# Kernel tuning notes

Hardware: AMD Instinct MI355X
Metric: run time of the kernel (lower is better)

Reference implementation:

```python
import jax, jax.numpy as jnp
import numpy as np

DIM = 1024
NUM_HEADS = 16
HEAD_DIM = DIM // NUM_HEADS


def apply_rotary_embed(x, thetas):
    # x: (..., seq, d), thetas: (seq, d) broadcast over leading dims
    x1, x2 = jnp.split(x, 2, axis=-1)
    x_rot = jnp.concatenate([-x2, x1], axis=-1)
    return x * jnp.cos(thetas) + x_rot * jnp.sin(thetas)


def setup_inputs() -> dict:
    key = jax.random.key(0)
    ks = jax.random.split(key, 8)
    B, Nx, Nc = 4, 1024, 2048
    x = jax.random.normal(ks[0], (B, Nx, DIM), dtype=jnp.float32)
    c = jax.random.normal(ks[1], (B, Nc, DIM), dtype=jnp.float32)
    x_pos_embed = jax.random.normal(ks[2], (Nx, HEAD_DIM), dtype=jnp.float32)
    c_pos_embed = jax.random.normal(ks[3], (Nc, HEAD_DIM), dtype=jnp.float32)
    s = 1.0 / np.sqrt(DIM)
    Wq = jax.random.normal(ks[4], (DIM, DIM), dtype=jnp.float32) * s
    Wkv = jax.random.normal(ks[5], (DIM, 2 * DIM), dtype=jnp.float32) * s
    Wproj = jax.random.normal(ks[6], (DIM, DIM), dtype=jnp.float32) * s
    bproj = jnp.zeros((DIM,), dtype=jnp.float32)
    return {"x": x, "c": c, "x_pos_embed": x_pos_embed, "c_pos_embed": c_pos_embed,
            "Wq": Wq, "Wkv": Wkv, "Wproj": Wproj, "bproj": bproj}


def reference(x, c, x_pos_embed, c_pos_embed, Wq, Wkv, Wproj, bproj):
    B, Nx, D = x.shape
    Nc = c.shape[1]
    H, hd = NUM_HEADS, HEAD_DIM
    # Q projection -> (B, H, Nx, hd)
    q = (x @ Wq).reshape(B, Nx, H, hd).transpose(0, 2, 1, 3)
    q = apply_rotary_embed(q, x_pos_embed)
    # KV projection -> k, v each (B, H, Nc, hd)
    kv = (c @ Wkv).reshape(B, Nc, 2, H, hd).transpose(2, 0, 3, 1, 4)
    k, v = kv[0], kv[1]
    k = apply_rotary_embed(k, c_pos_embed)
    # scaled dot-product attention (dropout p=0 -> identity)
    scale = 1.0 / np.sqrt(hd).astype(np.float32)
    attn = jnp.einsum('bhqd,bhkd->bhqk', q, k) * scale
    attn = jax.nn.softmax(attn, axis=-1)
    out = jnp.einsum('bhqk,bhkd->bhqd', attn, v)
    out = out.transpose(0, 2, 1, 3).reshape(B, Nx, D)
    return out @ Wproj + bproj
```

## Files before the change

kernel.cpp:

```cpp
#include <hip/hip_runtime.h>
#include <math.h>

#define DIMC  1024
#define NHEAD 16
#define HD    64
#define NB    4
#define NX    1024
#define NC    2048
#define KD    1024

typedef _Float16 half_t;
typedef __attribute__((ext_vector_type(8))) _Float16 h8;
typedef __attribute__((ext_vector_type(4))) _Float16 h4;
typedef __attribute__((ext_vector_type(2))) __fp16 fp16x2;
typedef __attribute__((ext_vector_type(4))) float f32x4;

#define QSCALE 0.1803368801111244f
#define NEGM  -8.656170245333781f

__device__ __forceinline__ void gload_lds16(const half_t* g, half_t* l) {
    __builtin_amdgcn_global_load_lds(
        (__attribute__((address_space(1))) void*)(g),
        (__attribute__((address_space(3))) void*)(l), 16, 0, 0);
}

__device__ __forceinline__ void wtile(const float* __restrict__ W,
                                      half_t* __restrict__ Wt, int N, int IMG,
                                      int bx, int by, int t)
{
    __shared__ half_t T[64][72];
    const int k0 = by * 64, n0 = bx * 64;
    const int kr = t >> 2, c0 = (t & 3) << 4;
    const float* src = W + (size_t)(k0 + kr) * N + n0 + c0;
#pragma unroll
    for (int j = 0; j < 16; j += 4) {
        float4 v = *(const float4*)(src + j);
        T[c0 + j + 0][kr] = (half_t)v.x;
        T[c0 + j + 1][kr] = (half_t)v.y;
        T[c0 + j + 2][kr] = (half_t)v.z;
        T[c0 + j + 3][kr] = (half_t)v.w;
    }
    __syncthreads();
    const int nr = t >> 2, kc = (t & 3) << 4;
    if (!IMG) {
        half_t* dst = Wt + (size_t)(n0 + nr) * KD + k0 + kc;
        *(int4*)dst       = *(const int4*)&T[nr][kc];
        *(int4*)(dst + 8) = *(const int4*)&T[nr][kc + 8];
    } else {
        const int n = n0 + nr;
        const int ntile = n >> 8, rr = n & 255;
        const int s0 = kc >> 3;
        half_t* base = Wt + ((size_t)(ntile * 16 + by) * 256 + rr) * 64;
        *(int4*)(base + ((s0 ^ (rr & 7)) << 3))       = *(const int4*)&T[nr][kc];
        *(int4*)(base + (((s0 + 1) ^ (rr & 7)) << 3)) = *(const int4*)&T[nr][kc + 8];
    }
}

__global__ __launch_bounds__(256) void prep(
    const float* __restrict__ x, half_t* __restrict__ xh,
    const float* __restrict__ c, half_t* __restrict__ ch,
    const float* __restrict__ xpe, const float* __restrict__ cpe,
    float* __restrict__ xct, float* __restrict__ xst,
    float* __restrict__ cct, float* __restrict__ cst,
    const float* __restrict__ Wq,  half_t* __restrict__ Wqt,
    const float* __restrict__ Wkv, half_t* __restrict__ Wkt,
    const float* __restrict__ Wp,  half_t* __restrict__ Wpt)
{
    const int bid = blockIdx.x, t = threadIdx.x;
    if (bid < 1024) {
        if (bid < 256)      wtile(Wq,  Wqt, DIMC, 0,     bid & 15,         bid >> 4,         t);
        else if (bid < 768) wtile(Wkv, Wkt, 2 * DIMC, 1, (bid - 256) & 31, (bid - 256) >> 5, t);
        else                wtile(Wp,  Wpt, DIMC, 0,     (bid - 768) & 15, (bid - 768) >> 4, t);
    } else if (bid < 7168) {
        const int nx = NB * NX * DIMC;
        const int i = ((bid - 1024) * 256 + t) * 8;
        const float* s;
        h8 o;
        if (i < nx) {
            s = x + i;
            float4 a = *(const float4*)(s);
            float4 b = *(const float4*)(s + 4);
            o[0] = (half_t)a.x; o[1] = (half_t)a.y; o[2] = (half_t)a.z; o[3] = (half_t)a.w;
            o[4] = (half_t)b.x; o[5] = (half_t)b.y; o[6] = (half_t)b.z; o[7] = (half_t)b.w;
            *(h8*)(xh + i) = o;
        } else {
            const int j = i - nx;
            s = c + j;
            float4 a = *(const float4*)(s);
            float4 b = *(const float4*)(s + 4);
            o[0] = (half_t)a.x; o[1] = (half_t)a.y; o[2] = (half_t)a.z; o[3] = (half_t)a.w;
            o[4] = (half_t)b.x; o[5] = (half_t)b.y; o[6] = (half_t)b.z; o[7] = (half_t)b.w;
            const int R = j >> 10, k = j & 1023;
            const int mt = R >> 8, r = R & 255, kt = k >> 6, sl = (k & 63) >> 3;
            *(h8*)(ch + ((size_t)(mt * 16 + kt) * 256 + r) * 64 + ((sl ^ (r & 7)) << 3)) = o;
        }
    } else {
        const int i = (bid - 7168) * 256 + t;
        if (i < NX * HD) {
            const float th = xpe[i];
            xct[i] = cosf(th); xst[i] = sinf(th);
        } else {
            const int j = i - NX * HD;
            const float th = cpe[j];
            cct[j] = cosf(th); cst[j] = sinf(th);
        }
    }
}

template <int MODE, int BN>
__global__ __launch_bounds__(256) void hgemm(
    const half_t* __restrict__ Ag, const half_t* __restrict__ Bt,
    const float* __restrict__ ct, const float* __restrict__ st,
    const float* __restrict__ bias,
    void* __restrict__ out0, void* __restrict__ out1)
{
    constexpr int MI = (BN == 128) ? 4 : 2;
    constexpr int BLOADS = BN / 32;
    __shared__ half_t As[2][8192];
    __shared__ half_t Bs[2][BN * 64];

    const int tid = threadIdx.x;
    const int w = tid >> 6, lane = tid & 63;
    const int lr = lane & 15, lg = lane >> 4;
    const int wrOff = (BN == 128) ? (w >> 1) * 64 : w * 32;
    const int wcOff = (BN == 128) ? (w & 1) * 64 : 0;

    int lin = (int)blockIdx.x;
    lin = (lin & 7) * ((int)gridDim.x >> 3) + (lin >> 3);
    const int m0 = (lin >> 4) * 128, n0 = (lin & 15) * BN;

    f32x4 acc[MI][4];
#pragma unroll
    for (int i = 0; i < MI; ++i)
#pragma unroll
        for (int j = 0; j < 4; ++j) acc[i][j] = f32x4{0.f, 0.f, 0.f, 0.f};

    size_t gA[4], gB[BLOADS];
    int loff[4];
#pragma unroll
    for (int c = 0; c < 4; ++c) {
        const int L = c * 4096 + w * 1024 + lane * 16;
        const int row = L >> 7;
        const int ss = ((L >> 4) & 7) ^ (row & 7);
        gA[c] = (size_t)(m0 + row) * KD + ss * 8;
        if (c < BLOADS) gB[c] = (size_t)(n0 + row) * KD + ss * 8;
        loff[c] = c * 2048 + w * 512;
    }

#define HSTAGE(buf, kk) do {                                               \
        _Pragma("unroll")                                                  \
        for (int c = 0; c < 4; ++c) {                                      \
            gload_lds16(Ag + gA[c] + (kk) * 64, &As[buf][loff[c]]);        \
            if (c < BLOADS) gload_lds16(Bt + gB[c] + (kk) * 64, &Bs[buf][loff[c]]); \
        }                                                                  \
    } while (0)

    HSTAGE(0, 0);
    asm volatile("s_waitcnt vmcnt(0)" ::: "memory");
    __builtin_amdgcn_s_barrier();
    __builtin_amdgcn_sched_barrier(0);

    for (int k = 0; k < KD / 64; ++k) {
        const int cb = k & 1;
        if (k + 1 < KD / 64) {
            HSTAGE(cb ^ 1, k + 1);
            if constexpr (BLOADS == 4)
                asm volatile("s_waitcnt vmcnt(8)" ::: "memory");
            else
                asm volatile("s_waitcnt vmcnt(6)" ::: "memory");
        } else {
            asm volatile("s_waitcnt vmcnt(0)" ::: "memory");
        }
        __builtin_amdgcn_s_barrier();
        __builtin_amdgcn_sched_barrier(0);

        __builtin_amdgcn_s_setprio(1);
#pragma unroll
        for (int kc = 0; kc < 2; ++kc) {
            h8 af[MI], bf[4];
#pragma unroll
            for (int mi = 0; mi < MI; ++mi) {
                const int r = wrOff + mi * 16 + lr;
                af[mi] = *(const h8*)&As[cb][r * 64 + (((kc * 4 + lg) ^ (r & 7)) << 3)];
            }
#pragma unroll
            for (int ni = 0; ni < 4; ++ni) {
                const int r = wcOff + ni * 16 + lr;
                bf[ni] = *(const h8*)&Bs[cb][r * 64 + (((kc * 4 + lg) ^ (r & 7)) << 3)];
            }
#pragma unroll
            for (int mi = 0; mi < MI; ++mi)
#pragma unroll
                for (int ni = 0; ni < 4; ++ni)
                    acc[mi][ni] = __builtin_amdgcn_mfma_f32_16x16x32_f16(
                        af[mi], bf[ni], acc[mi][ni], 0, 0, 0);
        }
        __builtin_amdgcn_s_setprio(0);

        __builtin_amdgcn_s_barrier();
        __builtin_amdgcn_sched_barrier(0);
    }
#undef HSTAGE

    if (MODE == 2) {
        float* o = (float*)out0;
#pragma unroll
        for (int ni = 0; ni < 4; ++ni) {
            const int col = n0 + ni * 16 + lr;
            const float bv = bias[col];
#pragma unroll
            for (int mi = 0; mi < MI; ++mi)
#pragma unroll
                for (int r = 0; r < 4; ++r) {
                    const int row = m0 + wrOff + mi * 16 + lg * 4 + r;
                    o[(size_t)row * DIMC + col] = acc[mi][ni][r] + bv;
                }
        }
        return;
    }

    if (MODE == 0) {
        half_t* Qw = (half_t*)out0;
        const int h = n0 >> 6;
#pragma unroll
        for (int mi = 0; mi < MI; ++mi)
#pragma unroll
            for (int r = 0; r < 4; ++r) {
                const int row = m0 + wrOff + mi * 16 + lg * 4 + r;
                const int bb = row >> 10, nn = row & (NX - 1);
                const float* cr = ct + nn * HD;
                const float* sr = st + nn * HD;
                half_t* op = Qw + (((size_t)(bb * NHEAD + h)) * NX + nn) * HD;
#pragma unroll
                for (int ni = 0; ni < 4; ++ni) {
                    const int d = ni * 16 + lr;
                    const float val = acc[mi][ni][r];
                    const float pv  = acc[mi][ni ^ 2][r];
                    op[d] = (half_t)((val * cr[d] + (ni < 2 ? -pv : pv) * sr[d]) * QSCALE);
                }
            }
    }
}

__global__ __launch_bounds__(512, 2) void hgemm_kv(
    const half_t* __restrict__ Aimg, const half_t* __restrict__ Bimg,
    const float* __restrict__ ct, const float* __restrict__ st,
    half_t* __restrict__ Kw, half_t* __restrict__ Vw)
{
    __shared__ half_t lds[65536];

    const int tid = threadIdx.x;
    const int w = tid >> 6, lane = tid & 63;
    const int lr = lane & 15, lg = lane >> 4;
    const int wr = w >> 2, wc = w & 3;
    const int wrOff = wr * 128, wcOff = wc * 64;

    int lin = (int)blockIdx.x;
    lin = (lin & 7) * 32 + (lin >> 3);
    const int mt = lin >> 3, nt = lin & 7;
    const int m0 = mt * 256, n0 = nt * 256;

    const half_t* Ablk = Aimg + (size_t)mt * 262144;
    const half_t* Bblk = Bimg + (size_t)nt * 262144;
    const int so2 = w * 512 + lane * 8;

    f32x4 acc[8][4];
#pragma unroll
    for (int i = 0; i < 8; ++i)
#pragma unroll
        for (int j = 0; j < 4; ++j) acc[i][j] = f32x4{0.f, 0.f, 0.f, 0.f};
    h8 af[2][2];
    h8 bf[4][2];

#define ISSUEH(SRC, DSTOFF) do {                                     \
        gload_lds16((SRC) + so2,        &lds[(DSTOFF) + w * 512]);   \
        gload_lds16((SRC) + 4096 + so2, &lds[(DSTOFF) + 4096 + w * 512]); \
    } while (0)

#define PHASE(MI0, AOFF, BOFF, READBF, STG, GATE) do {               \
        _Pragma("unroll")                                            \
        for (int kc = 0; kc < 2; ++kc)                               \
        _Pragma("unroll")                                            \
        for (int d = 0; d < 2; ++d) {                                \
            const int r_ = wrOff + ((MI0) + d) * 16 + lr;            \
            af[d][kc] = *(const h8*)&lds[(AOFF) + r_ * 64 + (((kc * 4 + lg) ^ (r_ & 7)) << 3)]; \
        }                                                            \
        if (READBF) {                                                \
            _Pragma("unroll")                                        \
            for (int ni = 0; ni < 4; ++ni)                           \
            _Pragma("unroll")                                        \
            for (int kc = 0; kc < 2; ++kc) {                         \
                const int rb = wcOff + ni * 16 + lr;                 \
                bf[ni][kc] = *(const h8*)&lds[(BOFF) + rb * 64 + (((kc * 4 + lg) ^ (rb & 7)) << 3)]; \
            }                                                        \
        }                                                            \
        STG;                                                         \
        __builtin_amdgcn_sched_barrier(0);                           \
        __builtin_amdgcn_s_barrier();                                \
        __builtin_amdgcn_s_setprio(1);                               \
        _Pragma("unroll")                                            \
        for (int d = 0; d < 2; ++d)                                  \
        _Pragma("unroll")                                            \
        for (int ni = 0; ni < 4; ++ni)                               \
        _Pragma("unroll")                                            \
        for (int kc = 0; kc < 2; ++kc)                               \
            acc[(MI0) + d][ni] = __builtin_amdgcn_mfma_f32_16x16x32_f16( \
                af[d][kc], bf[ni][kc], acc[(MI0) + d][ni], 0, 0, 0); \
        __builtin_amdgcn_s_setprio(0);                               \
        GATE;                                                        \
        __builtin_amdgcn_s_barrier();                                \
    } while (0)

#define GATE4 asm volatile("s_waitcnt vmcnt(4)" ::: "memory")
#define GATE0 asm volatile("s_waitcnt vmcnt(0)" ::: "memory")
#define NOG   ((void)0)

    ISSUEH(Ablk, 0);          ISSUEH(Ablk + 8192, 8192);
    ISSUEH(Bblk, 32768);      ISSUEH(Bblk + 8192, 32768 + 8192);
    __builtin_amdgcn_sched_barrier(0);
    ISSUEH(Bblk + 16384, 49152); ISSUEH(Bblk + 16384 + 8192, 49152 + 8192);
    asm volatile("s_waitcnt vmcnt(4)" ::: "memory");
    __builtin_amdgcn_s_barrier();

    for (int i = 0; i < 7; ++i) {
        const half_t* An1 = Ablk + (size_t)(2 * i + 1) * 16384;
        const half_t* An2 = Ablk + (size_t)(2 * i + 2) * 16384;
        const half_t* Bn2 = Bblk + (size_t)(2 * i + 2) * 16384;
        const half_t* Bn3 = Bblk + (size_t)(2 * i + 3) * 16384;
        PHASE(0, 0,     32768, true,  ISSUEH(An1, 16384),               NOG);
        PHASE(2, 0,     32768, false, ISSUEH(An1 + 8192, 16384 + 8192), NOG);
        PHASE(4, 0,     32768, false, ISSUEH(Bn2, 32768),               NOG);
        PHASE(6, 0,     32768, false, ISSUEH(Bn2 + 8192, 32768 + 8192), GATE4);
        PHASE(0, 16384, 49152, true,  ISSUEH(An2, 0),                   NOG);
        PHASE(2, 16384, 49152, false, ISSUEH(An2 + 8192, 8192),         NOG);
        PHASE(4, 16384, 49152, false, ISSUEH(Bn3, 49152),               NOG);
        PHASE(6, 16384, 49152, false, ISSUEH(Bn3 + 8192, 49152 + 8192), GATE4);
    }
    {
        const half_t* A15 = Ablk + (size_t)15 * 16384;
        PHASE(0, 0,     32768, true,  ISSUEH(A15, 16384),               NOG);
        PHASE(2, 0,     32768, false, ISSUEH(A15 + 8192, 16384 + 8192), NOG);
        PHASE(4, 0,     32768, false, NOG,                              NOG);
        PHASE(6, 0,     32768, false, NOG,                              GATE0);
        PHASE(0, 16384, 49152, true,  NOG,                              NOG);
        PHASE(2, 16384, 49152, false, NOG,                              NOG);
        PHASE(4, 16384, 49152, false, NOG,                              NOG);
        PHASE(6, 16384, 49152, false, NOG,                              NOG);
    }
#undef PHASE
#undef ISSUEH
#undef GATE4
#undef GATE0
#undef NOG

    const bool isK = (n0 < DIMC);
    const int h = ((n0 & (DIMC - 1)) >> 6) + wc;
#pragma unroll
    for (int mi = 0; mi < 8; ++mi)
#pragma unroll
        for (int r = 0; r < 4; ++r) {
            const int row = m0 + wrOff + mi * 16 + lg * 4 + r;
            const int bb = row >> 11, nn = row & (NC - 1);
            const int tt = nn >> 6, rr = nn & 63;
            const size_t tbase = ((size_t)(bb * NHEAD + h) * 32 + tt) * 4096;
            const float* cr = ct + nn * HD;
            const float* sr = st + nn * HD;
#pragma unroll
            for (int ni = 0; ni < 4; ++ni) {
                const int d = ni * 16 + lr;
                const float val = acc[mi][ni][r];
                if (isK) {
                    const float pv = acc[mi][ni ^ 2][r];
                    Kw[tbase + rr * 64 + ((((d >> 3) ^ (rr & 7)) << 3) | (d & 7))] =
                        (half_t)(val * cr[d] + (ni < 2 ? -pv : pv) * sr[d]);
                } else {
                    Vw[tbase + d * 64 + ((((rr >> 3) ^ (d & 7)) << 3) | (rr & 7))] =
                        (half_t)val;
                }
            }
        }
}

__global__ __launch_bounds__(256) void attn_mfma(
    const half_t* __restrict__ Q, const half_t* __restrict__ Kg,
    const half_t* __restrict__ Vg, half_t* __restrict__ O)
{
    __shared__ half_t Ks[2][4096];
    __shared__ half_t Vs[2][4096];
    __shared__ half_t Ps[4096];

    const int tid = threadIdx.x;
    const int w = tid >> 6, lane = tid & 63;
    const int lr = lane & 15, lg = lane >> 4;
    const int e7 = lr & 7;

    const int sid = (blockIdx.x & 7) * 128 + (blockIdx.x >> 3);
    const int bh = sid >> 4;
    const int q0 = (sid & 15) * 64;
    const int b = bh >> 4, h = bh & 15;

    const half_t* qbase = Q + ((size_t)bh * NX + q0 + w * 16 + lr) * HD + lg * 8;
    const h8 qf0 = *(const h8*)(qbase);
    const h8 qf1 = *(const h8*)(qbase + 32);

    f32x4 acc[4];
#pragma unroll
    for (int i = 0; i < 4; ++i) acc[i] = f32x4{0.f, 0.f, 0.f, 0.f};
    f32x4 accl = {0.f, 0.f, 0.f, 0.f};

    h8 vone;
#pragma unroll
    for (int i = 0; i < 8; ++i) vone[i] = (half_t)(lr == 0 ? 1.0f : 0.0f);

    const half_t* Kt = Kg + (size_t)bh * 32 * 4096;
    const half_t* Vt = Vg + (size_t)bh * 32 * 4096;
    const int so = w * 512 + lane * 8;

#define STAGE(bi, t) do {                                           \
        const half_t* kg_ = Kt + (size_t)(t) * 4096;                \
        const half_t* vg_ = Vt + (size_t)(t) * 4096;                \
        gload_lds16(kg_ + so,        &Ks[bi][w * 512]);             \
        gload_lds16(kg_ + 2048 + so, &Ks[bi][2048 + w * 512]);      \
        gload_lds16(vg_ + so,        &Vs[bi][w * 512]);             \
        gload_lds16(vg_ + 2048 + so, &Vs[bi][2048 + w * 512]);      \
    } while (0)

    STAGE(0, 0);
    asm volatile("s_waitcnt vmcnt(0)" ::: "memory");
    __builtin_amdgcn_s_barrier();
    __builtin_amdgcn_sched_barrier(0);

    const int rowq = w * 16 + lr;

    for (int t = 0; t < NC / 64; ++t) {
        const int cur = t & 1;
        if (t + 1 < NC / 64) {
            STAGE(cur ^ 1, t + 1);
            asm volatile("s_waitcnt vmcnt(8)" ::: "memory");
        } else {
            asm volatile("s_waitcnt vmcnt(0)" ::: "memory");
        }
        __builtin_amdgcn_s_barrier();
        __builtin_amdgcn_sched_barrier(0);

        f32x4 sc[4];
        __builtin_amdgcn_s_setprio(1);
#pragma unroll
        for (int cb = 0; cb < 4; ++cb) {
            const int r = cb * 16 + lr;
            const h8 kf0 = *(const h8*)&Ks[cur][r * 64 + ((lg ^ e7) << 3)];
            const h8 kf1 = *(const h8*)&Ks[cur][r * 64 + (((4 + lg) ^ e7) << 3)];
            f32x4 a = {NEGM, NEGM, NEGM, NEGM};
            a = __builtin_amdgcn_mfma_f32_16x16x32_f16(kf0, qf0, a, 0, 0, 0);
            a = __builtin_amdgcn_mfma_f32_16x16x32_f16(kf1, qf1, a, 0, 0, 0);
            sc[cb] = a;
        }
        __builtin_amdgcn_s_setprio(0);

#pragma unroll
        for (int cb = 0; cb < 4; ++cb) {
            fp16x2 a01 = __builtin_amdgcn_cvt_pkrtz(exp2f(sc[cb][0]), exp2f(sc[cb][1]));
            fp16x2 a23 = __builtin_amdgcn_cvt_pkrtz(exp2f(sc[cb][2]), exp2f(sc[cb][3]));
            union { h4 h; uint2 u; } pw;
            pw.u.x = *(unsigned int*)&a01;
            pw.u.y = *(unsigned int*)&a23;
            const int s = cb * 2 + (lg >> 1);
            *(h4*)&Ps[rowq * 64 + ((s ^ e7) << 3) + (lg & 1) * 4] = pw.h;
        }

        const h8 pf0 = *(const h8*)&Ps[rowq * 64 + ((lg ^ e7) << 3)];
        const h8 pf1 = *(const h8*)&Ps[rowq * 64 + (((4 + lg) ^ e7) << 3)];
        __builtin_amdgcn_s_setprio(1);
#pragma unroll
        for (int db = 0; db < 4; ++db) {
            const int rd = db * 16 + lr;
            const h8 vf0 = *(const h8*)&Vs[cur][rd * 64 + ((lg ^ e7) << 3)];
            const h8 vf1 = *(const h8*)&Vs[cur][rd * 64 + (((4 + lg) ^ e7) << 3)];
            acc[db] = __builtin_amdgcn_mfma_f32_16x16x32_f16(pf0, vf0, acc[db], 0, 0, 0);
            acc[db] = __builtin_amdgcn_mfma_f32_16x16x32_f16(pf1, vf1, acc[db], 0, 0, 0);
        }
        accl = __builtin_amdgcn_mfma_f32_16x16x32_f16(pf0, vone, accl, 0, 0, 0);
        accl = __builtin_amdgcn_mfma_f32_16x16x32_f16(pf1, vone, accl, 0, 0, 0);
        __builtin_amdgcn_s_setprio(0);

        __builtin_amdgcn_s_barrier();
        __builtin_amdgcn_sched_barrier(0);
    }
#undef STAGE

    float invs[4];
#pragma unroll
    for (int r = 0; r < 4; ++r)
        invs[r] = 1.f / __shfl(accl[r], lg << 4);

    half_t* Ob = O + ((size_t)b * NX + q0 + w * 16) * DIMC + h * HD;
#pragma unroll
    for (int db = 0; db < 4; ++db)
#pragma unroll
        for (int r = 0; r < 4; ++r)
            Ob[(size_t)(lg * 4 + r) * DIMC + db * 16 + lr] =
                (half_t)(acc[db][r] * invs[r]);
}

extern "C" void kernel_launch(void* const* d_in, const int* in_sizes, int n_in,
                              void* d_out, int out_size, void* d_ws, size_t ws_size,
                              hipStream_t stream)
{
    const float* x     = (const float*)d_in[0];
    const float* c     = (const float*)d_in[1];
    const float* xpe   = (const float*)d_in[2];
    const float* cpe   = (const float*)d_in[3];
    const float* Wq    = (const float*)d_in[4];
    const float* Wkv   = (const float*)d_in[5];
    const float* Wproj = (const float*)d_in[6];
    const float* bproj = (const float*)d_in[7];

    char* wsb = (char*)d_ws;
    half_t* xh  = (half_t*)(wsb);
    half_t* ch  = (half_t*)(wsb + ((size_t)8  << 20));
    half_t* Wqt = (half_t*)(wsb + ((size_t)24 << 20));
    half_t* Wkt = (half_t*)(wsb + ((size_t)26 << 20));
    half_t* Wpt = (half_t*)(wsb + ((size_t)30 << 20));
    half_t* Kw  = (half_t*)(wsb + ((size_t)32 << 20));
    half_t* Vw  = (half_t*)(wsb + ((size_t)48 << 20));
    half_t* Ow  = (half_t*)(wsb + ((size_t)64 << 20));
    float*  xct = (float*)(wsb + ((size_t)72 << 20));
    float*  xst = (float*)(wsb + ((size_t)72 << 20) + (256u << 10));
    float*  cct = (float*)(wsb + ((size_t)72 << 20) + (512u << 10));
    float*  cst = (float*)(wsb + ((size_t)72 << 20) + (1024u << 10));
    half_t* Qw  = (half_t*)d_out;

    prep<<<7936, 256, 0, stream>>>(x, xh, c, ch, xpe, cpe,
                                   xct, xst, cct, cst,
                                   Wq, Wqt, Wkv, Wkt, Wproj, Wpt);

    hgemm<0, 64><<<512, 256, 0, stream>>>(xh, Wqt, xct, xst, nullptr,
                                          Qw, nullptr);
    hgemm_kv<<<256, 512, 0, stream>>>(ch, Wkt, cct, cst, Kw, Vw);
    attn_mfma<<<1024, 256, 0, stream>>>(Qw, Kw, Vw, Ow);
    hgemm<2, 64><<<512, 256, 0, stream>>>(Ow, Wpt, nullptr, nullptr, bproj,
                                          (float*)d_out, nullptr);
}
```

Before: 184.8 us.

## Process 128 query rows per attention block to reuse K/V tiles

```diff
diff --git a/kernel.cpp b/kernel.cpp
--- a/kernel.cpp
+++ b/kernel.cpp
@@ -387,26 +387,30 @@
 {
     __shared__ half_t Ks[2][4096];
     __shared__ half_t Vs[2][4096];
-    __shared__ half_t Ps[4096];
+    __shared__ half_t Ps[8192];
 
     const int tid = threadIdx.x;
     const int w = tid >> 6, lane = tid & 63;
     const int lr = lane & 15, lg = lane >> 4;
     const int e7 = lr & 7;
 
-    const int sid = (blockIdx.x & 7) * 128 + (blockIdx.x >> 3);
-    const int bh = sid >> 4;
-    const int q0 = (sid & 15) * 64;
+    const int sid = (blockIdx.x & 7) * 64 + (blockIdx.x >> 3);
+    const int bh = sid >> 3;
+    const int q0 = (sid & 7) * 128;
     const int b = bh >> 4, h = bh & 15;
 
     const half_t* qbase = Q + ((size_t)bh * NX + q0 + w * 16 + lr) * HD + lg * 8;
-    const h8 qf0 = *(const h8*)(qbase);
-    const h8 qf1 = *(const h8*)(qbase + 32);
-
-    f32x4 acc[4];
-#pragma unroll
-    for (int i = 0; i < 4; ++i) acc[i] = f32x4{0.f, 0.f, 0.f, 0.f};
-    f32x4 accl = {0.f, 0.f, 0.f, 0.f};
+    const h8 qf0a = *(const h8*)(qbase);
+    const h8 qf1a = *(const h8*)(qbase + 32);
+    const h8 qf0b = *(const h8*)(qbase + (size_t)64 * HD);
+    const h8 qf1b = *(const h8*)(qbase + (size_t)64 * HD + 32);
+
+    f32x4 acc[2][4];
+#pragma unroll
+    for (int qb = 0; qb < 2; ++qb)
+#pragma unroll
+        for (int i = 0; i < 4; ++i) acc[qb][i] = f32x4{0.f, 0.f, 0.f, 0.f};
+    f32x4 accl[2] = {{0.f, 0.f, 0.f, 0.f}, {0.f, 0.f, 0.f, 0.f}};
 
     h8 vone;
 #pragma unroll
@@ -443,44 +447,68 @@
         __builtin_amdgcn_s_barrier();
         __builtin_amdgcn_sched_barrier(0);
 
-        f32x4 sc[4];
-        __builtin_amdgcn_s_setprio(1);
+        h8 kfr[4][2];
 #pragma unroll
         for (int cb = 0; cb < 4; ++cb) {
             const int r = cb * 16 + lr;
-            const h8 kf0 = *(const h8*)&Ks[cur][r * 64 + ((lg ^ e7) << 3)];
-            const h8 kf1 = *(const h8*)&Ks[cur][r * 64 + (((4 + lg) ^ e7) << 3)];
-            f32x4 a = {NEGM, NEGM, NEGM, NEGM};
-            a = __builtin_amdgcn_mfma_f32_16x16x32_f16(kf0, qf0, a, 0, 0, 0);
-            a = __builtin_amdgcn_mfma_f32_16x16x32_f16(kf1, qf1, a, 0, 0, 0);
-            sc[cb] = a;
-        }
-        __builtin_amdgcn_s_setprio(0);
-
-#pragma unroll
-        for (int cb = 0; cb < 4; ++cb) {
-            fp16x2 a01 = __builtin_amdgcn_cvt_pkrtz(exp2f(sc[cb][0]), exp2f(sc[cb][1]));
-            fp16x2 a23 = __builtin_amdgcn_cvt_pkrtz(exp2f(sc[cb][2]), exp2f(sc[cb][3]));
-            union { h4 h; uint2 u; } pw;
-            pw.u.x = *(unsigned int*)&a01;
-            pw.u.y = *(unsigned int*)&a23;
-            const int s = cb * 2 + (lg >> 1);
-            *(h4*)&Ps[rowq * 64 + ((s ^ e7) << 3) + (lg & 1) * 4] = pw.h;
-        }
-
-        const h8 pf0 = *(const h8*)&Ps[rowq * 64 + ((lg ^ e7) << 3)];
-        const h8 pf1 = *(const h8*)&Ps[rowq * 64 + (((4 + lg) ^ e7) << 3)];
+            kfr[cb][0] = *(const h8*)&Ks[cur][r * 64 + ((lg ^ e7) << 3)];
+            kfr[cb][1] = *(const h8*)&Ks[cur][r * 64 + (((4 + lg) ^ e7) << 3)];
+        }
+
+#pragma unroll
+        for (int qb = 0; qb < 2; ++qb) {
+            const h8 q0f = qb ? qf0b : qf0a;
+            const h8 q1f = qb ? qf1b : qf1a;
+            const int rowp = qb * 64 + rowq;
+
+            f32x4 sc[4];
+            __builtin_amdgcn_s_setprio(1);
+#pragma unroll
+            for (int cb = 0; cb < 4; ++cb) {
+                f32x4 a = {NEGM, NEGM, NEGM, NEGM};
+                a = __builtin_amdgcn_mfma_f32_16x16x32_f16(kfr[cb][0], q0f, a, 0, 0, 0);
+                a = __builtin_amdgcn_mfma_f32_16x16x32_f16(kfr[cb][1], q1f, a, 0, 0, 0);
+                sc[cb] = a;
+            }
+            __builtin_amdgcn_s_setprio(0);
+
+#pragma unroll
+            for (int cb = 0; cb < 4; ++cb) {
+                fp16x2 a01 = __builtin_amdgcn_cvt_pkrtz(exp2f(sc[cb][0]), exp2f(sc[cb][1]));
+                fp16x2 a23 = __builtin_amdgcn_cvt_pkrtz(exp2f(sc[cb][2]), exp2f(sc[cb][3]));
+                union { h4 h; uint2 u; } pw;
+                pw.u.x = *(unsigned int*)&a01;
+                pw.u.y = *(unsigned int*)&a23;
+                const int s = cb * 2 + (lg >> 1);
+                *(h4*)&Ps[rowp * 64 + ((s ^ e7) << 3) + (lg & 1) * 4] = pw.h;
+            }
+        }
+
+        h8 pf[2][2];
+#pragma unroll
+        for (int qb = 0; qb < 2; ++qb) {
+            const int rowp = qb * 64 + rowq;
+            pf[qb][0] = *(const h8*)&Ps[rowp * 64 + ((lg ^ e7) << 3)];
+            pf[qb][1] = *(const h8*)&Ps[rowp * 64 + (((4 + lg) ^ e7) << 3)];
+        }
+
         __builtin_amdgcn_s_setprio(1);
 #pragma unroll
         for (int db = 0; db < 4; ++db) {
             const int rd = db * 16 + lr;
             const h8 vf0 = *(const h8*)&Vs[cur][rd * 64 + ((lg ^ e7) << 3)];
             const h8 vf1 = *(const h8*)&Vs[cur][rd * 64 + (((4 + lg) ^ e7) << 3)];
-            acc[db] = __builtin_amdgcn_mfma_f32_16x16x32_f16(pf0, vf0, acc[db], 0, 0, 0);
-            acc[db] = __builtin_amdgcn_mfma_f32_16x16x32_f16(pf1, vf1, acc[db], 0, 0, 0);
-        }
-        accl = __builtin_amdgcn_mfma_f32_16x16x32_f16(pf0, vone, accl, 0, 0, 0);
-        accl = __builtin_amdgcn_mfma_f32_16x16x32_f16(pf1, vone, accl, 0, 0, 0);
+#pragma unroll
+            for (int qb = 0; qb < 2; ++qb) {
+                acc[qb][db] = __builtin_amdgcn_mfma_f32_16x16x32_f16(pf[qb][0], vf0, acc[qb][db], 0, 0, 0);
+                acc[qb][db] = __builtin_amdgcn_mfma_f32_16x16x32_f16(pf[qb][1], vf1, acc[qb][db], 0, 0, 0);
+            }
+        }
+#pragma unroll
+        for (int qb = 0; qb < 2; ++qb) {
+            accl[qb] = __builtin_amdgcn_mfma_f32_16x16x32_f16(pf[qb][0], vone, accl[qb], 0, 0, 0);
+            accl[qb] = __builtin_amdgcn_mfma_f32_16x16x32_f16(pf[qb][1], vone, accl[qb], 0, 0, 0);
+        }
         __builtin_amdgcn_s_setprio(0);
 
         __builtin_amdgcn_s_barrier();
@@ -488,18 +516,20 @@
     }
 #undef STAGE
 
-    float invs[4];
-#pragma unroll
-    for (int r = 0; r < 4; ++r)
-        invs[r] = 1.f / __shfl(accl[r], lg << 4);
-
     half_t* Ob = O + ((size_t)b * NX + q0 + w * 16) * DIMC + h * HD;
 #pragma unroll
-    for (int db = 0; db < 4; ++db)
+    for (int qb = 0; qb < 2; ++qb) {
+        float invs[4];
 #pragma unroll
         for (int r = 0; r < 4; ++r)
-            Ob[(size_t)(lg * 4 + r) * DIMC + db * 16 + lr] =
-                (half_t)(acc[db][r] * invs[r]);
+            invs[r] = 1.f / __shfl(accl[qb][r], lg << 4);
+#pragma unroll
+        for (int db = 0; db < 4; ++db)
+#pragma unroll
+            for (int r = 0; r < 4; ++r)
+                Ob[(size_t)(qb * 64 + lg * 4 + r) * DIMC + db * 16 + lr] =
+                    (half_t)(acc[qb][db][r] * invs[r]);
+    }
 }
 
 extern "C" void kernel_launch(void* const* d_in, const int* in_sizes, int n_in,
@@ -537,7 +567,7 @@
     hgemm<0, 64><<<512, 256, 0, stream>>>(xh, Wqt, xct, xst, nullptr,
                                           Qw, nullptr);
     hgemm_kv<<<256, 512, 0, stream>>>(ch, Wkt, cct, cst, Kw, Vw);
-    attn_mfma<<<1024, 256, 0, stream>>>(Qw, Kw, Vw, Ow);
+    attn_mfma<<<512, 256, 0, stream>>>(Qw, Kw, Vw, Ow);
     hgemm<2, 64><<<512, 256, 0, stream>>>(Ow, Wpt, nullptr, nullptr, bproj,
                                           (float*)d_out, nullptr);
 }
```

New measurement: 183.3 us. No clear change (-0.8%).

## Split attention KV range in two and add a combine kernel

Applied to the files above, without the earlier changes.

```diff
diff --git a/kernel.cpp b/kernel.cpp
--- a/kernel.cpp
+++ b/kernel.cpp
@@ -383,7 +383,8 @@
 
 __global__ __launch_bounds__(256) void attn_mfma(
     const half_t* __restrict__ Q, const half_t* __restrict__ Kg,
-    const half_t* __restrict__ Vg, half_t* __restrict__ O)
+    const half_t* __restrict__ Vg,
+    float* __restrict__ Opart, float* __restrict__ Lpart)
 {
     __shared__ half_t Ks[2][4096];
     __shared__ half_t Vs[2][4096];
@@ -394,10 +395,11 @@
     const int lr = lane & 15, lg = lane >> 4;
     const int e7 = lr & 7;
 
-    const int sid = (blockIdx.x & 7) * 128 + (blockIdx.x >> 3);
+    const int inner = (int)blockIdx.x & 1023;
+    const int kvh = (int)blockIdx.x >> 10;
+    const int sid = (inner & 7) * 128 + (inner >> 3);
     const int bh = sid >> 4;
     const int q0 = (sid & 15) * 64;
-    const int b = bh >> 4, h = bh & 15;
 
     const half_t* qbase = Q + ((size_t)bh * NX + q0 + w * 16 + lr) * HD + lg * 8;
     const h8 qf0 = *(const h8*)(qbase);
@@ -415,6 +417,7 @@
     const half_t* Kt = Kg + (size_t)bh * 32 * 4096;
     const half_t* Vt = Vg + (size_t)bh * 32 * 4096;
     const int so = w * 512 + lane * 8;
+    const int t0 = kvh * 16, t1 = t0 + 16;
 
 #define STAGE(bi, t) do {                                           \
         const half_t* kg_ = Kt + (size_t)(t) * 4096;                \
@@ -425,16 +428,16 @@
         gload_lds16(vg_ + 2048 + so, &Vs[bi][2048 + w * 512]);      \
     } while (0)
 
-    STAGE(0, 0);
+    STAGE(0, t0);
     asm volatile("s_waitcnt vmcnt(0)" ::: "memory");
     __builtin_amdgcn_s_barrier();
     __builtin_amdgcn_sched_barrier(0);
 
     const int rowq = w * 16 + lr;
 
-    for (int t = 0; t < NC / 64; ++t) {
+    for (int t = t0; t < t1; ++t) {
         const int cur = t & 1;
-        if (t + 1 < NC / 64) {
+        if (t + 1 < t1) {
             STAGE(cur ^ 1, t + 1);
             asm volatile("s_waitcnt vmcnt(8)" ::: "memory");
         } else {
@@ -488,18 +491,54 @@
     }
 #undef STAGE
 
-    float invs[4];
-#pragma unroll
-    for (int r = 0; r < 4; ++r)
-        invs[r] = 1.f / __shfl(accl[r], lg << 4);
-
-    half_t* Ob = O + ((size_t)b * NX + q0 + w * 16) * DIMC + h * HD;
+    const int slot = sid * 2 + kvh;
+    float* Po = Opart + (size_t)slot * 4096;
 #pragma unroll
     for (int db = 0; db < 4; ++db)
 #pragma unroll
         for (int r = 0; r < 4; ++r)
-            Ob[(size_t)(lg * 4 + r) * DIMC + db * 16 + lr] =
-                (half_t)(acc[db][r] * invs[r]);
+            Po[(w * 16 + lg * 4 + r) * 64 + db * 16 + lr] = acc[db][r];
+    if (lr == 0) {
+#pragma unroll
+        for (int r = 0; r < 4; ++r)
+            Lpart[(size_t)slot * 64 + w * 16 + lg * 4 + r] = accl[r];
+    }
+}
+
+__global__ __launch_bounds__(256) void combine(
+    const float* __restrict__ Opart, const float* __restrict__ Lpart,
+    half_t* __restrict__ Ow)
+{
+    const int pidx = blockIdx.x;
+    const int bh = pidx >> 4, qblk = pidx & 15;
+    const int b = bh >> 4, h = bh & 15;
+    const int t = threadIdx.x;
+    const int row = t >> 2;
+    const int c0 = (t & 3) << 4;
+
+    const float* P0 = Opart + (size_t)(pidx * 2 + 0) * 4096 + row * 64 + c0;
+    const float* P1 = Opart + (size_t)(pidx * 2 + 1) * 4096 + row * 64 + c0;
+    const float inv = 1.f / (Lpart[(size_t)(pidx * 2 + 0) * 64 + row] +
+                             Lpart[(size_t)(pidx * 2 + 1) * 64 + row]);
+
+    half_t* o = Ow + ((size_t)b * NX + qblk * 64 + row) * DIMC + h * 64 + c0;
+#pragma unroll
+    for (int j = 0; j < 16; j += 8) {
+        float4 a0 = *(const float4*)(P0 + j);
+        float4 a1 = *(const float4*)(P0 + j + 4);
+        float4 b0 = *(const float4*)(P1 + j);
+        float4 b1 = *(const float4*)(P1 + j + 4);
+        h8 ov;
+        ov[0] = (half_t)((a0.x + b0.x) * inv);
+        ov[1] = (half_t)((a0.y + b0.y) * inv);
+        ov[2] = (half_t)((a0.z + b0.z) * inv);
+        ov[3] = (half_t)((a0.w + b0.w) * inv);
+        ov[4] = (half_t)((a1.x + b1.x) * inv);
+        ov[5] = (half_t)((a1.y + b1.y) * inv);
+        ov[6] = (half_t)((a1.z + b1.z) * inv);
+        ov[7] = (half_t)((a1.w + b1.w) * inv);
+        *(h8*)(o + j) = ov;
+    }
 }
 
 extern "C" void kernel_launch(void* const* d_in, const int* in_sizes, int n_in,
@@ -520,7 +559,6 @@
     half_t* ch  = (half_t*)(wsb + ((size_t)8  << 20));
     half_t* Wqt = (half_t*)(wsb + ((size_t)24 << 20));
     half_t* Wkt = (half_t*)(wsb + ((size_t)26 << 20));
-    half_t* Wpt = (half_t*)(wsb + ((size_t)30 << 20));
     half_t* Kw  = (half_t*)(wsb + ((size_t)32 << 20));
     half_t* Vw  = (half_t*)(wsb + ((size_t)48 << 20));
     half_t* Ow  = (half_t*)(wsb + ((size_t)64 << 20));
@@ -528,6 +566,9 @@
     float*  xst = (float*)(wsb + ((size_t)72 << 20) + (256u << 10));
     float*  cct = (float*)(wsb + ((size_t)72 << 20) + (512u << 10));
     float*  cst = (float*)(wsb + ((size_t)72 << 20) + (1024u << 10));
+    half_t* Wpt = (half_t*)(wsb + ((size_t)74 << 20));
+    float*  Lpart = (float*)(wsb + ((size_t)76 << 20));
+    float*  Opart = (float*)(wsb);
     half_t* Qw  = (half_t*)d_out;
 
     prep<<<7936, 256, 0, stream>>>(x, xh, c, ch, xpe, cpe,
@@ -537,7 +578,8 @@
     hgemm<0, 64><<<512, 256, 0, stream>>>(xh, Wqt, xct, xst, nullptr,
                                           Qw, nullptr);
     hgemm_kv<<<256, 512, 0, stream>>>(ch, Wkt, cct, cst, Kw, Vw);
-    attn_mfma<<<1024, 256, 0, stream>>>(Qw, Kw, Vw, Ow);
+    attn_mfma<<<2048, 256, 0, stream>>>(Qw, Kw, Vw, Opart, Lpart);
+    combine<<<1024, 256, 0, stream>>>(Opart, Lpart, Ow);
     hgemm<2, 64><<<512, 256, 0, stream>>>(Ow, Wpt, nullptr, nullptr, bproj,
                                           (float*)d_out, nullptr);
 }
```

New measurement: 187.9 us. About the same (+1.7%).
